# Kernel optimization log

Hardware: AMD Instinct MI355X
Metric: run time of the kernel (lower is better)

Reference implementation:

```python
import jax, jax.numpy as jnp
import numpy as np
from jax import lax

D_MODEL = 1024
H = 16
D_K = D_MODEL // H
B = 2
S = 1024


def _conv3x3(x, w, b):
    # x: [B, C_in, S, S], w: [C_out, C_in, 3, 3], b: [C_out]; SAME padding=1
    y = lax.conv_general_dilated(x, w, window_strides=(1, 1),
                                 padding=((1, 1), (1, 1)),
                                 dimension_numbers=("NCHW", "OIHW", "NCHW"))
    return y + b[None, :, None, None]


def setup_inputs() -> dict:
    key = jax.random.key(0)
    ks = jax.random.split(key, 12)
    q = jax.random.normal(ks[0], (B, S, D_MODEL), dtype=jnp.float32)
    k = jax.random.normal(ks[1], (B, S, D_MODEL), dtype=jnp.float32)
    v = jax.random.normal(ks[2], (B, S, D_MODEL), dtype=jnp.float32)
    mask = jax.random.randint(ks[3], (B, S), 0, 2, dtype=jnp.int32)
    prev = jax.random.normal(ks[4], (B, H, S, S), dtype=jnp.float32)
    sc = 1.0 / np.sqrt(D_MODEL)
    Wq = jax.random.normal(ks[5], (D_MODEL, D_MODEL), dtype=jnp.float32) * sc
    Wk = jax.random.normal(ks[6], (D_MODEL, D_MODEL), dtype=jnp.float32) * sc
    Wv = jax.random.normal(ks[7], (D_MODEL, D_MODEL), dtype=jnp.float32) * sc
    Wo = jax.random.normal(ks[8], (D_MODEL, D_MODEL), dtype=jnp.float32) * sc
    csc = 1.0 / np.sqrt(H * 9)
    Wt = jax.random.normal(ks[9], (H, H, 3, 3), dtype=jnp.float32) * csc
    bt = jnp.zeros((H,), dtype=jnp.float32)
    Wa = jax.random.normal(ks[10], (H, 2 * H, 3, 3), dtype=jnp.float32) * csc
    ba = jnp.zeros((H,), dtype=jnp.float32)
    return {"q": q, "k": k, "v": v, "mask": mask,
            "previous_attention_scores": prev,
            "Wq": Wq, "Wk": Wk, "Wv": Wv, "Wo": Wo,
            "Wt": Wt, "bt": bt, "Wa": Wa, "ba": ba}


def reference(q, k, v, mask, previous_attention_scores,
              Wq, Wk, Wv, Wo, Wt, bt, Wa, ba):
    # Linear projections (torch Linear: x @ W.T), reshape to [B, H, S, D_K]
    def split_heads(x):
        return x.reshape(B, S, H, D_K).transpose(0, 2, 1, 3)
    query = split_heads(q @ Wq.T)
    key_ = split_heads(k @ Wk.T)
    value = split_heads(v @ Wv.T)

    # Raw (unscaled) scores: [B, H, S, S]
    M = jnp.einsum("bhsd,bhtd->bhst", query, key_)
    # Transmit conv on previous layer's attention scores (heads = channels)
    Mt = _conv3x3(previous_attention_scores, Wt, bt)
    # Aggregate conv over concatenated [M, Mt]: 2H -> H channels
    Ma = _conv3x3(jnp.concatenate((M, Mt), axis=1), Wa, ba)
    # NOTE: original scales by sqrt(d_model), not sqrt(d_k)
    A = jax.nn.softmax(Ma / jnp.sqrt(jnp.float32(D_MODEL)), axis=-1)
    # NOTE: original applies masked_fill(-1e9) AFTER softmax (faithful)
    A = jnp.where(mask[:, None, None, :] == 0, jnp.float32(-1e9), A)

    ctx = jnp.einsum("bhst,bhtd->bhsd", A, value)  # [B, H, S, D_K]
    ctx = ctx.transpose(0, 2, 1, 3).reshape(B, S, H * D_K)
    out = ctx @ Wo.T
    return out, A
```

## Files before the change

### kernel.cpp

```cpp
#include <hip/hip_runtime.h>

#define B_  2
#define S_  1024
#define H_  16
#define DK_ 64
#define D_  1024

static const size_t BSD  = (size_t)B_ * S_ * D_;
static const size_t BHSS = (size_t)B_ * H_ * S_ * S_;

typedef __attribute__((ext_vector_type(8))) short bf16x8;
typedef __attribute__((ext_vector_type(4))) float floatx4;

__device__ __forceinline__ unsigned short f2bf(float f) {
  unsigned u = __builtin_bit_cast(unsigned, f);
  unsigned r = (u + 0x7FFFu + ((u >> 16) & 1u)) >> 16;
  return (unsigned short)r;
}

__global__ __launch_bounds__(256) void cvt_bf16_kernel(
    const float* __restrict__ src, unsigned short* __restrict__ dst, int n4) {
  int i = (blockIdx.x << 8) + threadIdx.x;
  if (i >= n4) return;
  float4 v = ((const float4*)src)[i];
  ushort4 o;
  o.x = f2bf(v.x); o.y = f2bf(v.y); o.z = f2bf(v.z); o.w = f2bf(v.w);
  ((ushort4*)dst)[i] = o;
}

__global__ __launch_bounds__(256) void gemm_bf16_nt_kernel(
    const unsigned short* __restrict__ A, const unsigned short* __restrict__ Bw,
    void* __restrict__ Cout, int K, int Mcols, int bf16_out) {
  __shared__ short As[64 * 40];
  __shared__ short Bs[64 * 40];
  int tid = threadIdx.x;
  int lane = tid & 63, w = tid >> 6;
  int quad = lane >> 4, xn = lane & 15;
  int row0 = blockIdx.y << 6, col0 = blockIdx.x << 6;
  int rw = w & 1, cw = w >> 1;
  int srow = tid >> 2, sk = (tid & 3) << 3;
  const unsigned short* Ap = A + (size_t)(row0 + srow) * K + sk;
  const unsigned short* Bp = Bw + (size_t)(col0 + srow) * K + sk;
  floatx4 acc[2][2] = {};
  for (int k0 = 0; k0 < K; k0 += 32) {
    uint4 av = *(const uint4*)(Ap + k0);
    uint4 bv = *(const uint4*)(Bp + k0);
    *(uint4*)&As[srow * 40 + sk] = av;
    *(uint4*)&Bs[srow * 40 + sk] = bv;
    __syncthreads();
    bf16x8 af[2], bf[2];
#pragma unroll
    for (int rt = 0; rt < 2; ++rt)
      af[rt] = *(const bf16x8*)&As[(rw * 32 + rt * 16 + xn) * 40 + quad * 8];
#pragma unroll
    for (int ct = 0; ct < 2; ++ct)
      bf[ct] = *(const bf16x8*)&Bs[(cw * 32 + ct * 16 + xn) * 40 + quad * 8];
#pragma unroll
    for (int rt = 0; rt < 2; ++rt)
#pragma unroll
      for (int ct = 0; ct < 2; ++ct)
        acc[rt][ct] = __builtin_amdgcn_mfma_f32_16x16x32_bf16(
            af[rt], bf[ct], acc[rt][ct], 0, 0, 0);
    __syncthreads();
  }
#pragma unroll
  for (int rt = 0; rt < 2; ++rt)
#pragma unroll
    for (int ct = 0; ct < 2; ++ct) {
      int colg = col0 + cw * 32 + ct * 16 + xn;
#pragma unroll
      for (int r = 0; r < 4; ++r) {
        int rowg = row0 + rw * 32 + rt * 16 + quad * 4 + r;
        if (bf16_out)
          ((unsigned short*)Cout)[(size_t)rowg * Mcols + colg] = f2bf(acc[rt][ct][r]);
        else
          ((float*)Cout)[(size_t)rowg * Mcols + colg] = acc[rt][ct][r];
      }
    }
}

__global__ __launch_bounds__(256) void scores_mfma_kernel(
    const unsigned short* __restrict__ Q, const unsigned short* __restrict__ Km,
    unsigned short* __restrict__ Mo) {
  __shared__ short Qs[128 * 72];
  __shared__ short Ks[64 * 72];
  int z = blockIdx.z, b = z >> 4, h = z & 15;
  int col0 = blockIdx.x << 6, row0 = blockIdx.y << 7;
  int tid = threadIdx.x;
  int lane = tid & 63, w = tid >> 6;
  int quad = lane >> 4, xn = lane & 15;
  const unsigned short* Qb = Q + (size_t)b * S_ * D_ + h * DK_;
  const unsigned short* Kb = Km + (size_t)b * S_ * D_ + h * DK_;
  for (int idx = tid; idx < 1024; idx += 256) {
    int r = idx >> 3, k8 = (idx & 7) << 3;
    uint4 v = *(const uint4*)&Qb[(size_t)(row0 + r) * D_ + k8];
    *(uint4*)&Qs[r * 72 + k8] = v;
  }
  for (int idx = tid; idx < 512; idx += 256) {
    int r = idx >> 3, k8 = (idx & 7) << 3;
    uint4 v = *(const uint4*)&Kb[(size_t)(col0 + r) * D_ + k8];
    *(uint4*)&Ks[r * 72 + k8] = v;
  }
  __syncthreads();
  floatx4 acc[2][4] = {};
#pragma unroll
  for (int ks = 0; ks < 2; ++ks) {
    bf16x8 af[2], bf[4];
#pragma unroll
    for (int rt = 0; rt < 2; ++rt)
      af[rt] = *(const bf16x8*)&Qs[(w * 32 + rt * 16 + xn) * 72 + ks * 32 + quad * 8];
#pragma unroll
    for (int ct = 0; ct < 4; ++ct)
      bf[ct] = *(const bf16x8*)&Ks[(ct * 16 + xn) * 72 + ks * 32 + quad * 8];
#pragma unroll
    for (int rt = 0; rt < 2; ++rt)
#pragma unroll
      for (int ct = 0; ct < 4; ++ct)
        acc[rt][ct] = __builtin_amdgcn_mfma_f32_16x16x32_bf16(
            af[rt], bf[ct], acc[rt][ct], 0, 0, 0);
  }
  unsigned short* Mb = Mo + (size_t)z * S_ * S_;
#pragma unroll
  for (int rt = 0; rt < 2; ++rt)
#pragma unroll
    for (int ct = 0; ct < 4; ++ct) {
      int t = col0 + ct * 16 + xn;
#pragma unroll
      for (int r = 0; r < 4; ++r) {
        int s = row0 + w * 32 + rt * 16 + quad * 4 + r;
        Mb[(size_t)s * S_ + t] = f2bf(acc[rt][ct][r]);
      }
    }
}

__global__ __launch_bounds__(256) void repack16b_kernel(
    const unsigned short* __restrict__ src, unsigned short* __restrict__ dst) {
  int x = (blockIdx.x << 8) + threadIdx.x;
  int y = blockIdx.y, b = blockIdx.z;
  const unsigned short* sp = src + ((size_t)b * 16 * S_ + y) * S_ + x;
  unsigned short out[16];
#pragma unroll
  for (int c = 0; c < 16; ++c) out[c] = sp[(size_t)c << 20];
  unsigned short* dp = dst + (((size_t)b * S_ + y) * S_ + x) * 16;
  unsigned wds[8];
#pragma unroll
  for (int i = 0; i < 8; ++i)
    wds[i] = (unsigned)out[2 * i] | ((unsigned)out[2 * i + 1] << 16);
  uint4 v0 = {wds[0], wds[1], wds[2], wds[3]};
  uint4 v1 = {wds[4], wds[5], wds[6], wds[7]};
  *(uint4*)dp = v0;
  *((uint4*)dp + 1) = v1;
}

__global__ __launch_bounds__(256) void repack16_kernel(
    const float* __restrict__ src, unsigned short* __restrict__ dst) {
  int x = (blockIdx.x << 8) + threadIdx.x;
  int y = blockIdx.y, b = blockIdx.z;
  const float* sp = src + ((size_t)b * 16 * S_ + y) * S_ + x;
  unsigned short out[16];
#pragma unroll
  for (int c = 0; c < 16; ++c) out[c] = f2bf(sp[(size_t)c << 20]);
  unsigned short* dp = dst + (((size_t)b * S_ + y) * S_ + x) * 16;
  unsigned wds[8];
#pragma unroll
  for (int i = 0; i < 8; ++i)
    wds[i] = (unsigned)out[2 * i] | ((unsigned)out[2 * i + 1] << 16);
  uint4 v0 = {wds[0], wds[1], wds[2], wds[3]};
  uint4 v1 = {wds[4], wds[5], wds[6], wds[7]};
  *(uint4*)dp = v0;
  *((uint4*)dp + 1) = v1;
}

__global__ __launch_bounds__(256) void conv_t_mfma_kernel(
    const unsigned short* __restrict__ prevT, const float* __restrict__ Wt,
    const float* __restrict__ bt, unsigned short* __restrict__ Mtbf) {
  __shared__ short Xs[10 * 66 * 24];
  int b = blockIdx.z;
  int x0 = blockIdx.x << 6, y0 = blockIdx.y << 3;
  int tid = threadIdx.x;
  int lane = tid & 63, w = tid >> 6;
  int quad = lane >> 4, xn = lane & 15;

  for (int idx = tid; idx < 1320; idx += 256) {
    int y = idx / 132;
    int r = idx - y * 132;
    int px = r >> 1, half = r & 1;
    int gy = y0 + y - 1, gx = x0 + px - 1;
    uint4 val = {0u, 0u, 0u, 0u};
    if ((unsigned)gy < (unsigned)S_ && (unsigned)gx < (unsigned)S_) {
      const unsigned short* sp =
          prevT + (((size_t)b * S_ + gy) * S_ + gx) * 16 + half * 8;
      val = *(const uint4*)sp;
    }
    *(uint4*)&Xs[(y * 66 + px) * 24 + half * 8] = val;
  }

  int m = xn;
  bf16x8 afr[5];
#pragma unroll
  for (int p = 0; p < 5; ++p) {
#pragma unroll
    for (int j = 0; j < 8; ++j) {
      int k = quad * 8 + j;
      int t = 2 * p + (k >> 4);
      float wv = 0.f;
      if (t < 9) wv = Wt[(m * 16 + (k & 15)) * 9 + t];
      afr[p][j] = (short)f2bf(wv);
    }
  }
  int tdy[5], tdx[5];
#pragma unroll
  for (int p = 0; p < 5; ++p) {
    int t = 2 * p + (quad >> 1);
    if (t > 8) t = 8;
    tdy[p] = t / 3;
    tdx[p] = t - tdy[p] * 3;
  }
  float btl[4];
#pragma unroll
  for (int r = 0; r < 4; ++r) btl[r] = bt[quad * 4 + r];

  __syncthreads();

#pragma unroll
  for (int ry = 0; ry < 2; ++ry) {
    int yl = w * 2 + ry;
    int y = y0 + yl;
#pragma unroll
    for (int seg = 0; seg < 4; ++seg) {
      floatx4 acc = {0.f, 0.f, 0.f, 0.f};
#pragma unroll
      for (int p = 0; p < 5; ++p) {
        const short* bp =
            &Xs[((yl + tdy[p]) * 66 + seg * 16 + xn + tdx[p]) * 24 + (quad & 1) * 8];
        bf16x8 bfr = *(const bf16x8*)bp;
        acc = __builtin_amdgcn_mfma_f32_16x16x32_bf16(afr[p], bfr, acc, 0, 0, 0);
      }
      ushort4 pk;
      pk.x = f2bf(acc[0] + btl[0]);
      pk.y = f2bf(acc[1] + btl[1]);
      pk.z = f2bf(acc[2] + btl[2]);
      pk.w = f2bf(acc[3] + btl[3]);
      int gx = x0 + seg * 16 + xn;
      *(ushort4*)&Mtbf[(((size_t)b * S_ + y) * S_ + gx) * 16 + quad * 4] = pk;
    }
  }
}

__global__ __launch_bounds__(256) void conv_a_mfma_kernel(
    const unsigned short* __restrict__ Mbf, const unsigned short* __restrict__ Mtbf,
    const float* __restrict__ Wa, const float* __restrict__ ba,
    float* __restrict__ Y) {
  __shared__ short Xs[10 * 66 * 40];
  int b = blockIdx.z;
  int x0 = blockIdx.x << 6, y0 = blockIdx.y << 3;
  int tid = threadIdx.x;
  int lane = tid & 63, w = tid >> 6;
  int quad = lane >> 4, xn = lane & 15;

  for (int idx = tid; idx < 2640; idx += 256) {
    int y = idx / 264;
    int r = idx - y * 264;
    int px = r >> 2, part = r & 3;
    int gy = y0 + y - 1, gx = x0 + px - 1;
    uint4 val = {0u, 0u, 0u, 0u};
    if ((unsigned)gy < (unsigned)S_ && (unsigned)gx < (unsigned)S_) {
      const unsigned short* base = (part < 2) ? Mbf : Mtbf;
      const unsigned short* sp =
          base + (((size_t)b * S_ + gy) * S_ + gx) * 16 + (part & 1) * 8;
      val = *(const uint4*)sp;
    }
    *(uint4*)&Xs[(y * 66 + px) * 40 + part * 8] = val;
  }

  int m = xn;
  bf16x8 afr[9];
#pragma unroll
  for (int t = 0; t < 9; ++t) {
#pragma unroll
    for (int j = 0; j < 8; ++j) {
      int k = quad * 8 + j;
      afr[t][j] = (short)f2bf(Wa[(m * 32 + k) * 9 + t]);
    }
  }
  float bal[4];
#pragma unroll
  for (int r = 0; r < 4; ++r) bal[r] = ba[quad * 4 + r];

  __syncthreads();

#pragma unroll
  for (int ry = 0; ry < 2; ++ry) {
    int yl = w * 2 + ry;
    int y = y0 + yl;
#pragma unroll
    for (int seg = 0; seg < 4; ++seg) {
      floatx4 acc = {0.f, 0.f, 0.f, 0.f};
#pragma unroll
      for (int t = 0; t < 9; ++t) {
        const int dy = t / 3, dx = t - (t / 3) * 3;
        const short* bp =
            &Xs[((yl + dy) * 66 + seg * 16 + xn + dx) * 40 + quad * 8];
        bf16x8 bfr = *(const bf16x8*)bp;
        acc = __builtin_amdgcn_mfma_f32_16x16x32_bf16(afr[t], bfr, acc, 0, 0, 0);
      }
      int gx = x0 + seg * 16 + xn;
#pragma unroll
      for (int r = 0; r < 4; ++r) {
        int mo = quad * 4 + r;
        Y[(((size_t)b * 16 + mo) * S_ + y) * S_ + gx] = acc[r] + bal[r];
      }
    }
  }
}

__global__ __launch_bounds__(256) void softmax_mask_kernel(
    float* __restrict__ A, const int* __restrict__ mask) {
  __shared__ float redm[4], reds[4];
  int row = blockIdx.x;
  int b = row >> 14;
  float* rp = A + (size_t)row * S_;
  int tid = threadIdx.x;
  int t = tid << 2;
  float4 x = *(const float4*)&rp[t];
  const float sc = 1.0f / 32.0f;
  x.x *= sc; x.y *= sc; x.z *= sc; x.w *= sc;
  float m = fmaxf(fmaxf(x.x, x.y), fmaxf(x.z, x.w));
#pragma unroll
  for (int off = 32; off; off >>= 1) m = fmaxf(m, __shfl_down(m, off));
  int lane = tid & 63, w = tid >> 6;
  if (lane == 0) redm[w] = m;
  __syncthreads();
  m = fmaxf(fmaxf(redm[0], redm[1]), fmaxf(redm[2], redm[3]));
  float e0 = __expf(x.x - m), e1 = __expf(x.y - m);
  float e2 = __expf(x.z - m), e3 = __expf(x.w - m);
  float s = e0 + e1 + e2 + e3;
#pragma unroll
  for (int off = 32; off; off >>= 1) s += __shfl_down(s, off);
  if (lane == 0) reds[w] = s;
  __syncthreads();
  s = reds[0] + reds[1] + reds[2] + reds[3];
  float inv = 1.0f / s;
  const int* mb = mask + b * S_;
  float4 o;
  o.x = (mb[t + 0] == 0) ? -1e9f : e0 * inv;
  o.y = (mb[t + 1] == 0) ? -1e9f : e1 * inv;
  o.z = (mb[t + 2] == 0) ? -1e9f : e2 * inv;
  o.w = (mb[t + 3] == 0) ? -1e9f : e3 * inv;
  *(float4*)&rp[t] = o;
}

__global__ __launch_bounds__(256) void ctx_kernel(
    const float* __restrict__ A, const float* __restrict__ V,
    float* __restrict__ Ctx) {
  __shared__ float As[16][68];
  __shared__ float Vs[16][68];
  int z = blockIdx.y, b = z >> 4, h = z & 15;
  const float* Ab = A + (size_t)z * S_ * S_;
  const float* Vb = V + (size_t)b * S_ * D_ + h * DK_;
  float* Cb = Ctx + (size_t)b * S_ * D_ + h * DK_;
  int tid = threadIdx.x;
  int tx = tid & 15, ty = tid >> 4;
  int row0 = blockIdx.x << 6;
  int lrow = tid >> 2, lk = (tid & 3) << 2;
  int vt = tid >> 4, vd = (tid & 15) << 2;
  float acc[4][4] = {};
  for (int t0 = 0; t0 < S_; t0 += 16) {
    float4 a4 = *(const float4*)&Ab[(size_t)(row0 + lrow) * S_ + t0 + lk];
    As[lk + 0][lrow] = a4.x; As[lk + 1][lrow] = a4.y;
    As[lk + 2][lrow] = a4.z; As[lk + 3][lrow] = a4.w;
    float4 v4 = *(const float4*)&Vb[(size_t)(t0 + vt) * D_ + vd];
    *(float4*)&Vs[vt][vd] = v4;
    __syncthreads();
#pragma unroll
    for (int kk = 0; kk < 16; ++kk) {
      float4 av = *(const float4*)&As[kk][ty << 2];
      float4 bv = *(const float4*)&Vs[kk][tx << 2];
      float a_[4] = {av.x, av.y, av.z, av.w};
      float b_[4] = {bv.x, bv.y, bv.z, bv.w};
#pragma unroll
      for (int i = 0; i < 4; ++i)
#pragma unroll
        for (int j = 0; j < 4; ++j)
          acc[i][j] = fmaf(a_[i], b_[j], acc[i][j]);
    }
    __syncthreads();
  }
#pragma unroll
  for (int i = 0; i < 4; ++i) {
    float4 st = make_float4(acc[i][0], acc[i][1], acc[i][2], acc[i][3]);
    *(float4*)&Cb[(size_t)(row0 + (ty << 2) + i) * D_ + (tx << 2)] = st;
  }
}

__global__ __launch_bounds__(256) void gemm_nt_kernel(
    const float* __restrict__ A, const float* __restrict__ Bm,
    float* __restrict__ C, int K, int ldc) {
  __shared__ float As[16][68];
  __shared__ float Bs[16][68];
  int tid = threadIdx.x;
  int tx = tid & 15, ty = tid >> 4;
  int row0 = blockIdx.y << 6, col0 = blockIdx.x << 6;
  int lrow = tid >> 2;
  int lk = (tid & 3) << 2;
  const float* Ap = A + (size_t)(row0 + lrow) * K + lk;
  const float* Bp = Bm + (size_t)(col0 + lrow) * K + lk;
  float acc[4][4] = {};
  for (int k0 = 0; k0 < K; k0 += 16) {
    float4 a4 = *(const float4*)(Ap + k0);
    float4 b4 = *(const float4*)(Bp + k0);
    As[lk + 0][lrow] = a4.x; As[lk + 1][lrow] = a4.y;
    As[lk + 2][lrow] = a4.z; As[lk + 3][lrow] = a4.w;
    Bs[lk + 0][lrow] = b4.x; Bs[lk + 1][lrow] = b4.y;
    Bs[lk + 2][lrow] = b4.z; Bs[lk + 3][lrow] = b4.w;
    __syncthreads();
#pragma unroll
    for (int kk = 0; kk < 16; ++kk) {
      float4 av = *(const float4*)&As[kk][ty << 2];
      float4 bv = *(const float4*)&Bs[kk][tx << 2];
      float a_[4] = {av.x, av.y, av.z, av.w};
      float b_[4] = {bv.x, bv.y, bv.z, bv.w};
#pragma unroll
      for (int i = 0; i < 4; ++i)
#pragma unroll
        for (int j = 0; j < 4; ++j)
          acc[i][j] = fmaf(a_[i], b_[j], acc[i][j]);
    }
    __syncthreads();
  }
#pragma unroll
  for (int i = 0; i < 4; ++i) {
    float4 st = make_float4(acc[i][0], acc[i][1], acc[i][2], acc[i][3]);
    *(float4*)&C[(size_t)(row0 + (ty << 2) + i) * ldc + col0 + (tx << 2)] = st;
  }
}

extern "C" void kernel_launch(void* const* d_in, const int* in_sizes, int n_in,
                              void* d_out, int out_size, void* d_ws, size_t ws_size,
                              hipStream_t stream) {
  const float* q    = (const float*)d_in[0];
  const float* k    = (const float*)d_in[1];
  const float* v    = (const float*)d_in[2];
  const int*   mask = (const int*)d_in[3];
  const float* prev = (const float*)d_in[4];
  const float* Wq   = (const float*)d_in[5];
  const float* Wk   = (const float*)d_in[6];
  const float* Wv   = (const float*)d_in[7];
  const float* Wo   = (const float*)d_in[8];
  const float* Wt   = (const float*)d_in[9];
  const float* bt   = (const float*)d_in[10];
  const float* Wa   = (const float*)d_in[11];
  const float* ba   = (const float*)d_in[12];

  float* out0 = (float*)d_out;
  float* Aout = out0 + BSD;

  char* wsp = (char*)d_ws;
  unsigned short* X1  = (unsigned short*)wsp; wsp += BSD * 2;
  unsigned short* W1  = (unsigned short*)wsp; wsp += (size_t)D_ * D_ * 2;
  unsigned short* Qb  = (unsigned short*)wsp; wsp += BSD * 2;
  unsigned short* Kb  = (unsigned short*)wsp; wsp += BSD * 2;
  float* Vb           = (float*)wsp;          wsp += BSD * 4;
  float* ctx2         = (float*)wsp;          wsp += BSD * 4;
  unsigned short* Mp  = (unsigned short*)wsp; wsp += BHSS * 2;
  unsigned short* Mbf = (unsigned short*)wsp; wsp += BHSS * 2;
  unsigned short* Mtbf= (unsigned short*)wsp; wsp += BHSS * 2;
  unsigned short* prevT = Mp;

  dim3 blk(256);
  int n4x = (int)(BSD / 4);
  int n4w = (D_ * D_) / 4;
  dim3 gX((n4x + 255) / 256), gW((n4w + 255) / 256);
  dim3 gProjB(D_ / 64, (B_ * S_) / 64);

  hipLaunchKernelGGL(cvt_bf16_kernel, gW, blk, 0, stream, Wq, W1, n4w);
  hipLaunchKernelGGL(cvt_bf16_kernel, gX, blk, 0, stream, q, X1, n4x);
  hipLaunchKernelGGL(gemm_bf16_nt_kernel, gProjB, blk, 0, stream, X1, W1,
                     (void*)Qb, D_, D_, 1);
  hipLaunchKernelGGL(cvt_bf16_kernel, gW, blk, 0, stream, Wk, W1, n4w);
  hipLaunchKernelGGL(cvt_bf16_kernel, gX, blk, 0, stream, k, X1, n4x);
  hipLaunchKernelGGL(gemm_bf16_nt_kernel, gProjB, blk, 0, stream, X1, W1,
                     (void*)Kb, D_, D_, 1);
  hipLaunchKernelGGL(cvt_bf16_kernel, gW, blk, 0, stream, Wv, W1, n4w);
  hipLaunchKernelGGL(cvt_bf16_kernel, gX, blk, 0, stream, v, X1, n4x);
  hipLaunchKernelGGL(gemm_bf16_nt_kernel, gProjB, blk, 0, stream, X1, W1,
                     (void*)Vb, D_, D_, 0);

  dim3 gSc(S_ / 64, S_ / 128, B_ * H_);
  hipLaunchKernelGGL(scores_mfma_kernel, gSc, blk, 0, stream, Qb, Kb, Mp);

  dim3 gRep(S_ / 256, S_, B_);
  hipLaunchKernelGGL(repack16b_kernel, gRep, blk, 0, stream, Mp, Mbf);

  hipLaunchKernelGGL(repack16_kernel, gRep, blk, 0, stream, prev, prevT);

  dim3 gConv(S_ / 64, S_ / 8, B_);
  hipLaunchKernelGGL(conv_t_mfma_kernel, gConv, blk, 0, stream, prevT, Wt, bt, Mtbf);

  hipLaunchKernelGGL(conv_a_mfma_kernel, gConv, blk, 0, stream, Mbf, Mtbf, Wa, ba, Aout);

  hipLaunchKernelGGL(softmax_mask_kernel, dim3(B_ * H_ * S_), blk, 0, stream,
                     Aout, mask);

  dim3 gCtx(S_ / 64, B_ * H_);
  hipLaunchKernelGGL(ctx_kernel, gCtx, blk, 0, stream, Aout, Vb, ctx2);

  dim3 gProj(D_ / 64, (B_ * S_) / 64);
  hipLaunchKernelGGL(gemm_nt_kernel, gProj, blk, 0, stream, ctx2, Wo, out0, D_, D_);
}
```

Before: 760.3 us.

## Fuse aggregate conv with softmax, use bf16 MFMA for ctx and output projection

The aggregate conv now computes a whole 1024-wide row for all 16 heads per block and runs the softmax and mask in registers. This removes the separate softmax pass that re-read and re-wrote the full fp32 attention tensor. The ctx and output GEMMs move from fp32 FMA to bf16 MFMA, using a transposed bf16 V and a bf16 probability matrix with masked entries zeroed. The -1e9 masked contribution is added back as a rank-1 correction (masked column sums of V times Wo) in the output GEMM epilogue. This trades precision (bf16 probabilities and ctx) and extra small kernels for much less memory traffic and much faster matmuls.

```diff
diff --git a/kernel.cpp b/kernel.cpp
--- a/kernel.cpp
+++ b/kernel.cpp
@@ -30,7 +30,8 @@
 
 __global__ __launch_bounds__(256) void gemm_bf16_nt_kernel(
     const unsigned short* __restrict__ A, const unsigned short* __restrict__ Bw,
-    void* __restrict__ Cout, int K, int Mcols, int bf16_out) {
+    void* __restrict__ Cout, int K, int Mcols, int bf16_out,
+    const float* __restrict__ corr) {
   __shared__ short As[64 * 40];
   __shared__ short Bs[64 * 40];
   int tid = threadIdx.x;
@@ -73,8 +74,11 @@
         int rowg = row0 + rw * 32 + rt * 16 + quad * 4 + r;
         if (bf16_out)
           ((unsigned short*)Cout)[(size_t)rowg * Mcols + colg] = f2bf(acc[rt][ct][r]);
-        else
-          ((float*)Cout)[(size_t)rowg * Mcols + colg] = acc[rt][ct][r];
+        else {
+          float v = acc[rt][ct][r];
+          if (corr) v += corr[((rowg >> 10) << 10) + colg];
+          ((float*)Cout)[(size_t)rowg * Mcols + colg] = v;
+        }
       }
     }
 }
@@ -247,192 +251,236 @@
   }
 }
 
-__global__ __launch_bounds__(256) void conv_a_mfma_kernel(
+__global__ __launch_bounds__(256) void conv_a_softmax_kernel(
     const unsigned short* __restrict__ Mbf, const unsigned short* __restrict__ Mtbf,
     const float* __restrict__ Wa, const float* __restrict__ ba,
-    float* __restrict__ Y) {
-  __shared__ short Xs[10 * 66 * 40];
-  int b = blockIdx.z;
-  int x0 = blockIdx.x << 6, y0 = blockIdx.y << 3;
+    const int* __restrict__ mask,
+    float* __restrict__ Aout, unsigned short* __restrict__ P0) {
+  __shared__ __attribute__((aligned(16))) short Xs[3 * 132 * 40];
+  __shared__ float redm[4][4][4];
+  __shared__ float reds[4][4][4];
+  int y = ((blockIdx.x & 7) << 7) + (blockIdx.x >> 3);
+  int b = blockIdx.y;
   int tid = threadIdx.x;
   int lane = tid & 63, w = tid >> 6;
   int quad = lane >> 4, xn = lane & 15;
 
-  for (int idx = tid; idx < 2640; idx += 256) {
-    int y = idx / 264;
-    int r = idx - y * 264;
-    int px = r >> 2, part = r & 3;
-    int gy = y0 + y - 1, gx = x0 + px - 1;
-    uint4 val = {0u, 0u, 0u, 0u};
-    if ((unsigned)gy < (unsigned)S_ && (unsigned)gx < (unsigned)S_) {
-      const unsigned short* base = (part < 2) ? Mbf : Mtbf;
-      const unsigned short* sp =
-          base + (((size_t)b * S_ + gy) * S_ + gx) * 16 + (part & 1) * 8;
-      val = *(const uint4*)sp;
-    }
-    *(uint4*)&Xs[(y * 66 + px) * 40 + part * 8] = val;
-  }
-
-  int m = xn;
   bf16x8 afr[9];
 #pragma unroll
-  for (int t = 0; t < 9; ++t) {
-#pragma unroll
-    for (int j = 0; j < 8; ++j) {
-      int k = quad * 8 + j;
-      afr[t][j] = (short)f2bf(Wa[(m * 32 + k) * 9 + t]);
-    }
-  }
+  for (int t = 0; t < 9; ++t)
+#pragma unroll
+    for (int j = 0; j < 8; ++j)
+      afr[t][j] = (short)f2bf(Wa[(xn * 32 + quad * 8 + j) * 9 + t]);
   float bal[4];
 #pragma unroll
   for (int r = 0; r < 4; ++r) bal[r] = ba[quad * 4 + r];
 
-  __syncthreads();
-
-#pragma unroll
-  for (int ry = 0; ry < 2; ++ry) {
-    int yl = w * 2 + ry;
-    int y = y0 + yl;
-#pragma unroll
-    for (int seg = 0; seg < 4; ++seg) {
-      floatx4 acc = {0.f, 0.f, 0.f, 0.f};
+  floatx4 acc[8][2] = {};
+#pragma unroll
+  for (int ci = 0; ci < 8; ++ci) {
+    int x0 = ci << 7;
+    for (int idx = tid; idx < 1560; idx += 256) {
+      int ry = idx / 520;
+      int rem = idx - ry * 520;
+      int px = rem >> 2, part = rem & 3;
+      int gy = y + ry - 1, gx = x0 + px - 1;
+      uint4 val = {0u, 0u, 0u, 0u};
+      if ((unsigned)gy < (unsigned)S_ && (unsigned)gx < (unsigned)S_) {
+        const unsigned short* base = (part < 2) ? Mbf : Mtbf;
+        val = *(const uint4*)&base[(((size_t)b * S_ + gy) * S_ + gx) * 16 + (part & 1) * 8];
+      }
+      *(uint4*)&Xs[(ry * 132 + px) * 40 + part * 8] = val;
+    }
+    __syncthreads();
+#pragma unroll
+    for (int sub = 0; sub < 2; ++sub) {
+      int sp = (w * 2 + sub) * 16 + xn;
+      floatx4 a = acc[ci][sub];
 #pragma unroll
       for (int t = 0; t < 9; ++t) {
         const int dy = t / 3, dx = t - (t / 3) * 3;
-        const short* bp =
-            &Xs[((yl + dy) * 66 + seg * 16 + xn + dx) * 40 + quad * 8];
-        bf16x8 bfr = *(const bf16x8*)bp;
-        acc = __builtin_amdgcn_mfma_f32_16x16x32_bf16(afr[t], bfr, acc, 0, 0, 0);
-      }
-      int gx = x0 + seg * 16 + xn;
+        bf16x8 bfr = *(const bf16x8*)&Xs[(dy * 132 + sp + dx) * 40 + quad * 8];
+        a = __builtin_amdgcn_mfma_f32_16x16x32_bf16(afr[t], bfr, a, 0, 0, 0);
+      }
+      acc[ci][sub] = a;
+    }
+    __syncthreads();
+  }
+
+  const float sc = 1.0f / 32.0f;
+  float mx[4] = {-3.4e38f, -3.4e38f, -3.4e38f, -3.4e38f};
+#pragma unroll
+  for (int ci = 0; ci < 8; ++ci)
+#pragma unroll
+    for (int sub = 0; sub < 2; ++sub)
+#pragma unroll
+      for (int r = 0; r < 4; ++r) {
+        float v = (acc[ci][sub][r] + bal[r]) * sc;
+        acc[ci][sub][r] = v;
+        mx[r] = fmaxf(mx[r], v);
+      }
+#pragma unroll
+  for (int r = 0; r < 4; ++r) {
+    mx[r] = fmaxf(mx[r], __shfl_xor(mx[r], 1));
+    mx[r] = fmaxf(mx[r], __shfl_xor(mx[r], 2));
+    mx[r] = fmaxf(mx[r], __shfl_xor(mx[r], 4));
+    mx[r] = fmaxf(mx[r], __shfl_xor(mx[r], 8));
+  }
+  if (xn == 0) {
+#pragma unroll
+    for (int r = 0; r < 4; ++r) redm[w][quad][r] = mx[r];
+  }
+  __syncthreads();
+  float fm[4];
+#pragma unroll
+  for (int r = 0; r < 4; ++r)
+    fm[r] = fmaxf(fmaxf(redm[0][quad][r], redm[1][quad][r]),
+                  fmaxf(redm[2][quad][r], redm[3][quad][r]));
+  float sm[4] = {0.f, 0.f, 0.f, 0.f};
+#pragma unroll
+  for (int ci = 0; ci < 8; ++ci)
+#pragma unroll
+    for (int sub = 0; sub < 2; ++sub)
+#pragma unroll
+      for (int r = 0; r < 4; ++r) {
+        float e = __expf(acc[ci][sub][r] - fm[r]);
+        acc[ci][sub][r] = e;
+        sm[r] += e;
+      }
+#pragma unroll
+  for (int r = 0; r < 4; ++r) {
+    sm[r] += __shfl_xor(sm[r], 1);
+    sm[r] += __shfl_xor(sm[r], 2);
+    sm[r] += __shfl_xor(sm[r], 4);
+    sm[r] += __shfl_xor(sm[r], 8);
+  }
+  if (xn == 0) {
+#pragma unroll
+    for (int r = 0; r < 4; ++r) reds[w][quad][r] = sm[r];
+  }
+  __syncthreads();
+  float inv[4];
+#pragma unroll
+  for (int r = 0; r < 4; ++r)
+    inv[r] = 1.0f / (reds[0][quad][r] + reds[1][quad][r] +
+                     reds[2][quad][r] + reds[3][quad][r]);
+
+  const int* mb = mask + b * S_;
+#pragma unroll
+  for (int ci = 0; ci < 8; ++ci)
+#pragma unroll
+    for (int sub = 0; sub < 2; ++sub) {
+      int gx = (ci << 7) + (w * 2 + sub) * 16 + xn;
+      int mk = mb[gx];
 #pragma unroll
       for (int r = 0; r < 4; ++r) {
         int mo = quad * 4 + r;
-        Y[(((size_t)b * 16 + mo) * S_ + y) * S_ + gx] = acc[r] + bal[r];
-      }
-    }
-  }
-}
-
-__global__ __launch_bounds__(256) void softmax_mask_kernel(
-    float* __restrict__ A, const int* __restrict__ mask) {
-  __shared__ float redm[4], reds[4];
-  int row = blockIdx.x;
-  int b = row >> 14;
-  float* rp = A + (size_t)row * S_;
+        size_t oidx = (((size_t)(b * 16 + mo)) << 20) + ((size_t)y << 10) + gx;
+        float p = acc[ci][sub][r] * inv[r];
+        Aout[oidx] = mk ? p : -1e9f;
+        P0[oidx]  = mk ? f2bf(p) : (unsigned short)0;
+      }
+    }
+}
+
+__global__ __launch_bounds__(256) void vtrans_kernel(
+    const float* __restrict__ V, unsigned short* __restrict__ Vt) {
+  __shared__ unsigned short Ls[64][68];
+  int z = blockIdx.y, b = z >> 4, h = z & 15;
+  int t0 = blockIdx.x << 6;
   int tid = threadIdx.x;
-  int t = tid << 2;
-  float4 x = *(const float4*)&rp[t];
-  const float sc = 1.0f / 32.0f;
-  x.x *= sc; x.y *= sc; x.z *= sc; x.w *= sc;
-  float m = fmaxf(fmaxf(x.x, x.y), fmaxf(x.z, x.w));
-#pragma unroll
-  for (int off = 32; off; off >>= 1) m = fmaxf(m, __shfl_down(m, off));
-  int lane = tid & 63, w = tid >> 6;
-  if (lane == 0) redm[w] = m;
+  for (int idx = tid; idx < 1024; idx += 256) {
+    int t = idx >> 4, d = (idx & 15) << 2;
+    float4 v4 = *(const float4*)&V[((size_t)b * S_ + t0 + t) * D_ + h * 64 + d];
+    ushort4 u;
+    u.x = f2bf(v4.x); u.y = f2bf(v4.y); u.z = f2bf(v4.z); u.w = f2bf(v4.w);
+    *(ushort4*)&Ls[t][d] = u;
+  }
   __syncthreads();
-  m = fmaxf(fmaxf(redm[0], redm[1]), fmaxf(redm[2], redm[3]));
-  float e0 = __expf(x.x - m), e1 = __expf(x.y - m);
-  float e2 = __expf(x.z - m), e3 = __expf(x.w - m);
-  float s = e0 + e1 + e2 + e3;
-#pragma unroll
-  for (int off = 32; off; off >>= 1) s += __shfl_down(s, off);
-  if (lane == 0) reds[w] = s;
-  __syncthreads();
-  s = reds[0] + reds[1] + reds[2] + reds[3];
-  float inv = 1.0f / s;
+  for (int idx = tid; idx < 1024; idx += 256) {
+    int d = idx >> 4, tc = (idx & 15) << 2;
+    ushort4 u;
+    u.x = Ls[tc + 0][d]; u.y = Ls[tc + 1][d];
+    u.z = Ls[tc + 2][d]; u.w = Ls[tc + 3][d];
+    *(ushort4*)&Vt[((size_t)(h * 64 + d)) * 2048 + (size_t)b * S_ + t0 + tc] = u;
+  }
+}
+
+__global__ __launch_bounds__(256) void colsum_kernel(
+    const float* __restrict__ V, const int* __restrict__ mask,
+    float* __restrict__ cs) {
+  int b = blockIdx.y;
+  int d = (blockIdx.x << 8) + threadIdx.x;
   const int* mb = mask + b * S_;
-  float4 o;
-  o.x = (mb[t + 0] == 0) ? -1e9f : e0 * inv;
-  o.y = (mb[t + 1] == 0) ? -1e9f : e1 * inv;
-  o.z = (mb[t + 2] == 0) ? -1e9f : e2 * inv;
-  o.w = (mb[t + 3] == 0) ? -1e9f : e3 * inv;
-  *(float4*)&rp[t] = o;
-}
-
-__global__ __launch_bounds__(256) void ctx_kernel(
-    const float* __restrict__ A, const float* __restrict__ V,
-    float* __restrict__ Ctx) {
-  __shared__ float As[16][68];
-  __shared__ float Vs[16][68];
+  float s = 0.f;
+  for (int t = 0; t < S_; ++t) {
+    float v = V[((size_t)b * S_ + t) * D_ + d];
+    if (mb[t] == 0) s += v;
+  }
+  cs[b * D_ + d] = s;
+}
+
+__global__ __launch_bounds__(256) void corr_kernel(
+    const float* __restrict__ cs, const float* __restrict__ Wo,
+    float* __restrict__ corr) {
+  int b = blockIdx.y;
+  int j = (blockIdx.x << 6) + (threadIdx.x >> 2);
+  int part = threadIdx.x & 3;
+  const float* c = cs + b * D_ + part * 256;
+  const float* wr = Wo + (size_t)j * D_ + part * 256;
+  float s = 0.f;
+  for (int i = 0; i < 256; i += 4) {
+    float4 w4 = *(const float4*)&wr[i];
+    float4 c4 = *(const float4*)&c[i];
+    s = fmaf(w4.x, c4.x, s); s = fmaf(w4.y, c4.y, s);
+    s = fmaf(w4.z, c4.z, s); s = fmaf(w4.w, c4.w, s);
+  }
+  s += __shfl_xor(s, 1);
+  s += __shfl_xor(s, 2);
+  if (part == 0) corr[b * D_ + j] = -1e9f * s;
+}
+
+__global__ __launch_bounds__(256) void ctx_mfma_kernel(
+    const unsigned short* __restrict__ P0, const unsigned short* __restrict__ Vt,
+    unsigned short* __restrict__ Cbf) {
+  __shared__ __attribute__((aligned(16))) short Ps[64 * 72];
+  __shared__ __attribute__((aligned(16))) short Vs[64 * 72];
   int z = blockIdx.y, b = z >> 4, h = z & 15;
-  const float* Ab = A + (size_t)z * S_ * S_;
-  const float* Vb = V + (size_t)b * S_ * D_ + h * DK_;
-  float* Cb = Ctx + (size_t)b * S_ * D_ + h * DK_;
-  int tid = threadIdx.x;
-  int tx = tid & 15, ty = tid >> 4;
   int row0 = blockIdx.x << 6;
-  int lrow = tid >> 2, lk = (tid & 3) << 2;
-  int vt = tid >> 4, vd = (tid & 15) << 2;
-  float acc[4][4] = {};
-  for (int t0 = 0; t0 < S_; t0 += 16) {
-    float4 a4 = *(const float4*)&Ab[(size_t)(row0 + lrow) * S_ + t0 + lk];
-    As[lk + 0][lrow] = a4.x; As[lk + 1][lrow] = a4.y;
-    As[lk + 2][lrow] = a4.z; As[lk + 3][lrow] = a4.w;
-    float4 v4 = *(const float4*)&Vb[(size_t)(t0 + vt) * D_ + vd];
-    *(float4*)&Vs[vt][vd] = v4;
+  int tid = threadIdx.x, lane = tid & 63, w = tid >> 6;
+  int quad = lane >> 4, xn = lane & 15;
+  const unsigned short* Pb = P0 + (size_t)z * S_ * S_ + (size_t)row0 * S_;
+  const unsigned short* Vb = Vt + ((size_t)h * 64) * 2048 + (size_t)b * S_;
+  floatx4 acc[4] = {};
+  for (int k0 = 0; k0 < S_; k0 += 64) {
+    for (int idx = tid; idx < 512; idx += 256) {
+      int r = idx >> 3, c = (idx & 7) << 3;
+      *(uint4*)&Ps[r * 72 + c] = *(const uint4*)&Pb[(size_t)r * S_ + k0 + c];
+    }
+    for (int idx = tid; idx < 512; idx += 256) {
+      int r = idx >> 3, c = (idx & 7) << 3;
+      *(uint4*)&Vs[r * 72 + c] = *(const uint4*)&Vb[(size_t)r * 2048 + k0 + c];
+    }
     __syncthreads();
 #pragma unroll
-    for (int kk = 0; kk < 16; ++kk) {
-      float4 av = *(const float4*)&As[kk][ty << 2];
-      float4 bv = *(const float4*)&Vs[kk][tx << 2];
-      float a_[4] = {av.x, av.y, av.z, av.w};
-      float b_[4] = {bv.x, bv.y, bv.z, bv.w};
-#pragma unroll
-      for (int i = 0; i < 4; ++i)
-#pragma unroll
-        for (int j = 0; j < 4; ++j)
-          acc[i][j] = fmaf(a_[i], b_[j], acc[i][j]);
+    for (int ks = 0; ks < 2; ++ks) {
+      bf16x8 af = *(const bf16x8*)&Ps[(w * 16 + xn) * 72 + ks * 32 + quad * 8];
+#pragma unroll
+      for (int ct = 0; ct < 4; ++ct) {
+        bf16x8 bfv = *(const bf16x8*)&Vs[(ct * 16 + xn) * 72 + ks * 32 + quad * 8];
+        acc[ct] = __builtin_amdgcn_mfma_f32_16x16x32_bf16(af, bfv, acc[ct], 0, 0, 0);
+      }
     }
     __syncthreads();
   }
-#pragma unroll
-  for (int i = 0; i < 4; ++i) {
-    float4 st = make_float4(acc[i][0], acc[i][1], acc[i][2], acc[i][3]);
-    *(float4*)&Cb[(size_t)(row0 + (ty << 2) + i) * D_ + (tx << 2)] = st;
-  }
-}
-
-__global__ __launch_bounds__(256) void gemm_nt_kernel(
-    const float* __restrict__ A, const float* __restrict__ Bm,
-    float* __restrict__ C, int K, int ldc) {
-  __shared__ float As[16][68];
-  __shared__ float Bs[16][68];
-  int tid = threadIdx.x;
-  int tx = tid & 15, ty = tid >> 4;
-  int row0 = blockIdx.y << 6, col0 = blockIdx.x << 6;
-  int lrow = tid >> 2;
-  int lk = (tid & 3) << 2;
-  const float* Ap = A + (size_t)(row0 + lrow) * K + lk;
-  const float* Bp = Bm + (size_t)(col0 + lrow) * K + lk;
-  float acc[4][4] = {};
-  for (int k0 = 0; k0 < K; k0 += 16) {
-    float4 a4 = *(const float4*)(Ap + k0);
-    float4 b4 = *(const float4*)(Bp + k0);
-    As[lk + 0][lrow] = a4.x; As[lk + 1][lrow] = a4.y;
-    As[lk + 2][lrow] = a4.z; As[lk + 3][lrow] = a4.w;
-    Bs[lk + 0][lrow] = b4.x; Bs[lk + 1][lrow] = b4.y;
-    Bs[lk + 2][lrow] = b4.z; Bs[lk + 3][lrow] = b4.w;
-    __syncthreads();
-#pragma unroll
-    for (int kk = 0; kk < 16; ++kk) {
-      float4 av = *(const float4*)&As[kk][ty << 2];
-      float4 bv = *(const float4*)&Bs[kk][tx << 2];
-      float a_[4] = {av.x, av.y, av.z, av.w};
-      float b_[4] = {bv.x, bv.y, bv.z, bv.w};
-#pragma unroll
-      for (int i = 0; i < 4; ++i)
-#pragma unroll
-        for (int j = 0; j < 4; ++j)
-          acc[i][j] = fmaf(a_[i], b_[j], acc[i][j]);
-    }
-    __syncthreads();
-  }
-#pragma unroll
-  for (int i = 0; i < 4; ++i) {
-    float4 st = make_float4(acc[i][0], acc[i][1], acc[i][2], acc[i][3]);
-    *(float4*)&C[(size_t)(row0 + (ty << 2) + i) * ldc + col0 + (tx << 2)] = st;
-  }
+  unsigned short* Co = Cbf + ((size_t)b * S_) * D_ + h * 64;
+#pragma unroll
+  for (int ct = 0; ct < 4; ++ct)
+#pragma unroll
+    for (int r = 0; r < 4; ++r) {
+      int s = row0 + w * 16 + quad * 4 + r;
+      Co[(size_t)s * D_ + ct * 16 + xn] = f2bf(acc[ct][r]);
+    }
 }
 
 extern "C" void kernel_launch(void* const* d_in, const int* in_sizes, int n_in,
@@ -456,16 +504,20 @@
   float* Aout = out0 + BSD;
 
   char* wsp = (char*)d_ws;
-  unsigned short* X1  = (unsigned short*)wsp; wsp += BSD * 2;
-  unsigned short* W1  = (unsigned short*)wsp; wsp += (size_t)D_ * D_ * 2;
-  unsigned short* Qb  = (unsigned short*)wsp; wsp += BSD * 2;
-  unsigned short* Kb  = (unsigned short*)wsp; wsp += BSD * 2;
-  float* Vb           = (float*)wsp;          wsp += BSD * 4;
-  float* ctx2         = (float*)wsp;          wsp += BSD * 4;
-  unsigned short* Mp  = (unsigned short*)wsp; wsp += BHSS * 2;
-  unsigned short* Mbf = (unsigned short*)wsp; wsp += BHSS * 2;
-  unsigned short* Mtbf= (unsigned short*)wsp; wsp += BHSS * 2;
+  unsigned short* X1   = (unsigned short*)wsp; wsp += BSD * 2;
+  unsigned short* W1   = (unsigned short*)wsp; wsp += (size_t)D_ * D_ * 2;
+  unsigned short* Qb   = (unsigned short*)wsp; wsp += BSD * 2;
+  unsigned short* Kb   = (unsigned short*)wsp; wsp += BSD * 2;
+  float* Vb            = (float*)wsp;          wsp += BSD * 4;
+  unsigned short* Vtb  = (unsigned short*)wsp; wsp += BSD * 2;
+  unsigned short* ctx1 = (unsigned short*)wsp; wsp += BSD * 2;
+  float* cs            = (float*)wsp;          wsp += (size_t)B_ * D_ * 4;
+  float* corrb         = (float*)wsp;          wsp += (size_t)B_ * D_ * 4;
+  unsigned short* Mp   = (unsigned short*)wsp; wsp += BHSS * 2;
+  unsigned short* Mbf  = (unsigned short*)wsp; wsp += BHSS * 2;
+  unsigned short* Mtbf = (unsigned short*)wsp; wsp += BHSS * 2;
   unsigned short* prevT = Mp;
+  unsigned short* P0    = Mp;
 
   dim3 blk(256);
   int n4x = (int)(BSD / 4);
@@ -476,15 +528,21 @@
   hipLaunchKernelGGL(cvt_bf16_kernel, gW, blk, 0, stream, Wq, W1, n4w);
   hipLaunchKernelGGL(cvt_bf16_kernel, gX, blk, 0, stream, q, X1, n4x);
   hipLaunchKernelGGL(gemm_bf16_nt_kernel, gProjB, blk, 0, stream, X1, W1,
-                     (void*)Qb, D_, D_, 1);
+                     (void*)Qb, D_, D_, 1, (const float*)nullptr);
   hipLaunchKernelGGL(cvt_bf16_kernel, gW, blk, 0, stream, Wk, W1, n4w);
   hipLaunchKernelGGL(cvt_bf16_kernel, gX, blk, 0, stream, k, X1, n4x);
   hipLaunchKernelGGL(gemm_bf16_nt_kernel, gProjB, blk, 0, stream, X1, W1,
-                     (void*)Kb, D_, D_, 1);
+                     (void*)Kb, D_, D_, 1, (const float*)nullptr);
   hipLaunchKernelGGL(cvt_bf16_kernel, gW, blk, 0, stream, Wv, W1, n4w);
   hipLaunchKernelGGL(cvt_bf16_kernel, gX, blk, 0, stream, v, X1, n4x);
   hipLaunchKernelGGL(gemm_bf16_nt_kernel, gProjB, blk, 0, stream, X1, W1,
-                     (void*)Vb, D_, D_, 0);
+                     (void*)Vb, D_, D_, 0, (const float*)nullptr);
+  hipLaunchKernelGGL(cvt_bf16_kernel, gW, blk, 0, stream, Wo, W1, n4w);
+
+  hipLaunchKernelGGL(vtrans_kernel, dim3(S_ / 64, B_ * H_), blk, 0, stream, Vb, Vtb);
+  hipLaunchKernelGGL(colsum_kernel, dim3(D_ / 256, B_), blk, 0, stream,
+                     Vb, mask, cs);
+  hipLaunchKernelGGL(corr_kernel, dim3(D_ / 64, B_), blk, 0, stream, cs, Wo, corrb);
 
   dim3 gSc(S_ / 64, S_ / 128, B_ * H_);
   hipLaunchKernelGGL(scores_mfma_kernel, gSc, blk, 0, stream, Qb, Kb, Mp);
@@ -497,14 +555,13 @@
   dim3 gConv(S_ / 64, S_ / 8, B_);
   hipLaunchKernelGGL(conv_t_mfma_kernel, gConv, blk, 0, stream, prevT, Wt, bt, Mtbf);
 
-  hipLaunchKernelGGL(conv_a_mfma_kernel, gConv, blk, 0, stream, Mbf, Mtbf, Wa, ba, Aout);
-
-  hipLaunchKernelGGL(softmax_mask_kernel, dim3(B_ * H_ * S_), blk, 0, stream,
-                     Aout, mask);
-
-  dim3 gCtx(S_ / 64, B_ * H_);
-  hipLaunchKernelGGL(ctx_kernel, gCtx, blk, 0, stream, Aout, Vb, ctx2);
+  hipLaunchKernelGGL(conv_a_softmax_kernel, dim3(S_, B_), blk, 0, stream,
+                     Mbf, Mtbf, Wa, ba, mask, Aout, P0);
+
+  hipLaunchKernelGGL(ctx_mfma_kernel, dim3(S_ / 64, B_ * H_), blk, 0, stream,
+                     P0, Vtb, ctx1);
 
   dim3 gProj(D_ / 64, (B_ * S_) / 64);
-  hipLaunchKernelGGL(gemm_nt_kernel, gProj, blk, 0, stream, ctx2, Wo, out0, D_, D_);
-}
+  hipLaunchKernelGGL(gemm_bf16_nt_kernel, gProj, blk, 0, stream, ctx1, W1,
+                     (void*)out0, D_, D_, 0, (const float*)corrb);
+}
```

After: 829.4 us. 9.1% more time.
